# Performance work log

Measured on AMD Instinct MI355X. Metric: run time of the kernel, lower is better.

Reference implementation:

```python
import jax, jax.numpy as jnp
import numpy as np

B, T, D = 16, 4096, 256
CODEBOOK_SIZE = 1024
COMMITMENT = 1.0


def setup_inputs() -> dict:
    key = jax.random.key(0)
    kx, kc = jax.random.split(key)
    x = jax.random.normal(kx, (B, T, D), dtype=jnp.float32)
    codebook = jax.random.normal(kc, (CODEBOOK_SIZE, D), dtype=jnp.float32)
    return {"x": x, "codebook": codebook}


def reference(x, codebook):
    # x: [B, T, D] continuous latents; codebook: [K, D]
    flat = x.reshape(-1, x.shape[-1])  # [N, D]
    # does not affect argmin but is kept for faithfulness to torch.cdist-style math)
    x_sq = jnp.sum(flat * flat, axis=1, keepdims=True)            # [N, 1]
    c_sq = jnp.sum(codebook * codebook, axis=1)                   # [K]
    dist = x_sq - 2.0 * (flat @ codebook.T) + c_sq[None, :]       # [N, K]
    indices = jnp.argmin(dist, axis=1)                            # [N] int
    quantized = codebook[indices].reshape(x.shape)                # gather, [B, T, D]
    # commitment loss: encoder pulled toward (stopped) codes
    commit_loss = COMMITMENT * jnp.mean(
        (x - jax.lax.stop_gradient(quantized)) ** 2
    )
    # straight-through estimator
    out = x + jax.lax.stop_gradient(quantized - x)
    return out, indices.reshape(x.shape[:-1]), commit_loss
```

## Files before the change

kernel.cpp:

```cpp
#include <hip/hip_runtime.h>

#define N_TOK 65536
#define DIM   256
#define KCODE 1024

#define NTHREADS 256
#define TM 128
#define TN 128
#define BK 64
#define NCHUNK 8

#define REFINE_EPS 0.125f
#define TIE_THETA 1.0e-4

#define WS_CSQ_OFF   16
#define WS_IDX_OFF   2048
#define WS_PAIRS_OFF (WS_IDX_OFF + N_TOK)
#define WS_CBPK_OFF  (WS_PAIRS_OFF + N_TOK * NCHUNK * 4)

typedef float f32x4  __attribute__((ext_vector_type(4)));
typedef short bf16x8 __attribute__((ext_vector_type(8)));

__global__ void zero_loss_kernel(float* ws) {
    if (threadIdx.x == 0) ws[0] = 0.0f;
}

__global__ void rowsq_np_kernel(const float* __restrict__ m,
                                float* __restrict__ out, int rows) {
#pragma clang fp contract(off)
    int row = blockIdx.x * 16 + (threadIdx.x >> 4);
    int l   = threadIdx.x & 15;
    if (row >= rows) return;
    int h = l >> 3;
    int j = l & 7;
    const float* p = m + (size_t)row * DIM + h * 128 + j;
    float v = p[0];
    float r = v * v;
#pragma unroll
    for (int i = 1; i < 16; ++i) {
        float w  = p[i * 8];
        float w2 = w * w;
        r = r + w2;
    }
    float t = r + __shfl_xor(r, 1);
    t = t + __shfl_xor(t, 2);
    t = t + __shfl_xor(t, 4);
    t = t + __shfl_xor(t, 8);
    if (l == 0) out[row] = t;
}

__device__ __forceinline__ void ins2(float d, int idx,
                                     float& d1, int& i1, float& d2, int& i2) {
    if (d < d1 || (d == d1 && idx < i1)) {
        d2 = d1; i2 = i1; d1 = d; i1 = idx;
    } else if ((d < d2 || (d == d2 && idx < i2)) && idx != i1) {
        d2 = d; i2 = idx;
    }
}

__device__ __forceinline__ void f2bf_split(float v, short& hi, short& lo) {
    unsigned u = __float_as_uint(v);
    unsigned r = (u + 0x7fffu + ((u >> 16) & 1u)) >> 16;
    hi = (short)r;
    float hf = __uint_as_float(r << 16);
    float lf = v - hf;
    unsigned u2 = __float_as_uint(lf);
    unsigned r2 = (u2 + 0x7fffu + ((u2 >> 16) & 1u)) >> 16;
    lo = (short)r2;
}

__global__ void convert_pack_kernel(const float* __restrict__ src,
                                    unsigned short* __restrict__ dst,
                                    int nquads) {
    for (int i = blockIdx.x * blockDim.x + threadIdx.x; i < nquads;
         i += gridDim.x * blockDim.x) {
        int row = i >> 6;
        int kq  = i & 63;
        float4 v = reinterpret_cast<const float4*>(src)[i];
        short h0, l0, h1, l1, h2, l2, h3, l3;
        f2bf_split(v.x, h0, l0); f2bf_split(v.y, h1, l1);
        f2bf_split(v.z, h2, l2); f2bf_split(v.w, h3, l3);
        *reinterpret_cast<short4*>(dst + (size_t)row * 512 + kq * 4) =
            make_short4(h0, h1, h2, h3);
        *reinterpret_cast<short4*>(dst + (size_t)row * 512 + 256 + kq * 4) =
            make_short4(l0, l1, l2, l3);
    }
}

__device__ __forceinline__ void gload_lds16(const unsigned short* g, unsigned short* lds) {
    __builtin_amdgcn_global_load_lds(
        (const __attribute__((address_space(1))) unsigned int*)g,
        (__attribute__((address_space(3))) unsigned int*)lds, 16, 0, 0);
}

__launch_bounds__(NTHREADS, 2)
__global__ void vq_main_kernel(const unsigned short* __restrict__ xpk,
                               const unsigned short* __restrict__ cbpk,
                               const float* __restrict__ csq,
                               float4* __restrict__ pairs) {
    __shared__ __align__(16) unsigned short Atile[TM * BK];
    __shared__ __align__(16) unsigned short Btile[TN * BK];
    __shared__ __align__(16) float4 pairs_sh[TM][2];

    const int tid  = threadIdx.x;
    const int w    = tid >> 6;
    const int wy   = w >> 1;
    const int wx   = w & 1;
    const int lane = tid & 63;
    const int lm   = lane & 15;
    const int q    = lane >> 4;
    const int bx     = blockIdx.x;
    const int tok0   = (bx >> 3) * TM;
    const int cchunk = bx & 7;
    const int code0  = cchunk * TN;

    const int row_off = lane >> 3;
    const int slot    = lane & 7;
    const int kq      = slot ^ row_off;

    float cs_reg[4];
#pragma unroll
    for (int ni = 0; ni < 4; ++ni)
        cs_reg[ni] = csq[code0 + wx * 64 + ni * 16 + lm];

    f32x4 acc[4][4];
#pragma unroll
    for (int mi = 0; mi < 4; ++mi)
#pragma unroll
        for (int ni = 0; ni < 4; ++ni)
            acc[mi][ni] = (f32x4){0.f, 0.f, 0.f, 0.f};

    const int segA[3] = {0, 0, 256};
    const int segB[3] = {0, 256, 0};

#pragma unroll 1
    for (int seg = 0; seg < 3; ++seg) {
        const int sa = segA[seg], sb = segB[seg];
#pragma unroll 1
        for (int kc = 0; kc < DIM / BK; ++kc) {
            const int k0 = kc * BK;
            __syncthreads();
#pragma unroll
            for (int inst = 0; inst < 4; ++inst) {
                int rbase = w * 32 + inst * 8;
                const unsigned short* ga =
                    xpk + (size_t)(tok0 + rbase + row_off) * 512 + sa + k0 + kq * 8;
                gload_lds16(ga, &Atile[rbase * BK]);
                const unsigned short* gb =
                    cbpk + (size_t)(code0 + rbase + row_off) * 512 + sb + k0 + kq * 8;
                gload_lds16(gb, &Btile[rbase * BK]);
            }
            __syncthreads();

#pragma unroll
            for (int t = 0; t < 2; ++t) {
                bf16x8 af[4], bf[4];
#pragma unroll
                for (int mi = 0; mi < 4; ++mi) {
                    int r = wy * 64 + mi * 16 + lm;
                    af[mi] = *reinterpret_cast<const bf16x8*>(
                        &Atile[r * BK + (((t * 4 + q) ^ (r & 7)) * 8)]);
                }
#pragma unroll
                for (int ni = 0; ni < 4; ++ni) {
                    int r = wx * 64 + ni * 16 + lm;
                    bf[ni] = *reinterpret_cast<const bf16x8*>(
                        &Btile[r * BK + (((t * 4 + q) ^ (r & 7)) * 8)]);
                }
#pragma unroll
                for (int mi = 0; mi < 4; ++mi)
#pragma unroll
                    for (int ni = 0; ni < 4; ++ni)
                        acc[mi][ni] = __builtin_amdgcn_mfma_f32_16x16x32_bf16(
                            af[mi], bf[ni], acc[mi][ni], 0, 0, 0);
            }
        }
    }

#pragma unroll
    for (int mi = 0; mi < 4; ++mi) {
#pragma unroll
        for (int r = 0; r < 4; ++r) {
            int row_local = wy * 64 + mi * 16 + q * 4 + r;
            float l1 = 3.4e38f, l2 = 3.4e38f;
            int   j1 = 0x7fffffff, j2 = 0x7fffffff;
#pragma unroll
            for (int ni = 0; ni < 4; ++ni) {
                float d = cs_reg[ni] - 2.0f * acc[mi][ni][r];
                ins2(d, code0 + wx * 64 + ni * 16 + lm, l1, j1, l2, j2);
            }
#pragma unroll
            for (int m = 1; m < 16; m <<= 1) {
                float o1 = __shfl_xor(l1, m);
                int   p1 = __shfl_xor(j1, m);
                float o2 = __shfl_xor(l2, m);
                int   p2 = __shfl_xor(j2, m);
                ins2(o1, p1, l1, j1, l2, j2);
                ins2(o2, p2, l1, j1, l2, j2);
            }
            if (lm == 0) {
                float4 pr;
                pr.x = l1; pr.y = l2;
                pr.z = __int_as_float(j1); pr.w = __int_as_float(j2);
                pairs_sh[row_local][wx] = pr;
            }
        }
    }
    __syncthreads();
    if (tid < TM) {
        float4 pa = pairs_sh[tid][0];
        float4 pb = pairs_sh[tid][1];
        float d1 = pa.x, d2 = pa.y;
        int   i1 = __float_as_int(pa.z), i2 = __float_as_int(pa.w);
        ins2(pb.x, __float_as_int(pb.z), d1, i1, d2, i2);
        ins2(pb.y, __float_as_int(pb.w), d1, i1, d2, i2);
        float4 pr;
        pr.x = d1; pr.y = d2;
        pr.z = __int_as_float(i1); pr.w = __int_as_float(i2);
        pairs[(size_t)(tok0 + tid) * NCHUNK + cchunk] = pr;
    }
}

__global__ void merge_refine_kernel(const float* __restrict__ x,
                                    const float* __restrict__ cb,
                                    const float4* __restrict__ pairs,
                                    int* __restrict__ idx_out) {
    int t = blockIdx.x * 256 + threadIdx.x;
    if (t >= N_TOK) return;
    float4 p0 = pairs[(size_t)t * NCHUNK];
    float d1 = p0.x, d2 = p0.y;
    int   i1 = __float_as_int(p0.z), i2 = __float_as_int(p0.w);
#pragma unroll
    for (int c = 1; c < NCHUNK; ++c) {
        float4 p = pairs[(size_t)t * NCHUNK + c];
        ins2(p.x, __float_as_int(p.z), d1, i1, d2, i2);
        ins2(p.y, __float_as_int(p.w), d1, i1, d2, i2);
    }

    int pick = i1;
    if (d2 - d1 < REFINE_EPS) {
        const float* xr = x + (size_t)t * DIM;
        const float* c1 = cb + (size_t)i1 * DIM;
        const float* c2 = cb + (size_t)i2 * DIM;
        double sA = 0.0, dA = 0.0, sB = 0.0, dB = 0.0;
        for (int k = 0; k < DIM; ++k) {
            double xv = (double)xr[k];
            double a  = (double)c1[k];
            double b  = (double)c2[k];
            sA += a * a; dA += xv * a;
            sB += b * b; dB += xv * b;
        }
        double DA  = sA - 2.0 * dA;
        double DB  = sB - 2.0 * dB;
        double gap = DB - DA;
        if (gap > TIE_THETA)       pick = i1;
        else if (gap < -TIE_THETA) pick = i2;
        else                       pick = (i1 < i2) ? i1 : i2;
    }
    idx_out[t] = pick;
}

__launch_bounds__(NTHREADS)
__global__ void output_kernel(const float* __restrict__ x,
                              const float* __restrict__ cb,
                              const int* __restrict__ idx,
                              float* __restrict__ out_q,
                              float* __restrict__ out_idx,
                              float* __restrict__ loss_ws) {
    __shared__ int   sh_idx[TM];
    __shared__ float wsum[4];
    const int tid  = threadIdx.x;
    const int tok0 = blockIdx.x * TM;

    if (tid < TM) sh_idx[tid] = idx[tok0 + tid];
    __syncthreads();

    float lsum = 0.0f;
    for (int t = 0; t < TM; ++t) {
        int code = sh_idx[t];
        float qv = cb[(size_t)code * DIM + tid];
        float xv = x[(size_t)(tok0 + t) * DIM + tid];
        out_q[(size_t)(tok0 + t) * DIM + tid] = xv + (qv - xv);
        float df = xv - qv;
        lsum = fmaf(df, df, lsum);
    }
    if (tid < TM) out_idx[tok0 + tid] = (float)sh_idx[tid];

#pragma unroll
    for (int off = 1; off < 64; off <<= 1) lsum += __shfl_xor(lsum, off);
    if ((tid & 63) == 0) wsum[tid >> 6] = lsum;
    __syncthreads();
    if (tid == 0) atomicAdd(loss_ws, (wsum[0] + wsum[1]) + (wsum[2] + wsum[3]));
}

__global__ void finalize_kernel(const float* ws, float* out_loss) {
    if (threadIdx.x == 0) out_loss[0] = ws[0] * (1.0f / 16777216.0f);
}

extern "C" void kernel_launch(void* const* d_in, const int* in_sizes, int n_in,
                              void* d_out, int out_size, void* d_ws, size_t ws_size,
                              hipStream_t stream) {
    const float* x  = (const float*)d_in[0];
    const float* cb = (const float*)d_in[1];

    float* out      = (float*)d_out;
    float* out_q    = out;
    float* out_idx  = out + (size_t)N_TOK * DIM;
    float* out_loss = out_idx + N_TOK;

    float*  ws    = (float*)d_ws;
    float*  csq   = ws + WS_CSQ_OFF;
    int*    idx   = (int*)(ws + WS_IDX_OFF);
    float4* pairs = (float4*)(ws + WS_PAIRS_OFF);
    unsigned short* cbpk = (unsigned short*)(ws + WS_CBPK_OFF);
    unsigned short* xpk  = (unsigned short*)out_q;

    zero_loss_kernel<<<1, 64, 0, stream>>>(ws);
    rowsq_np_kernel<<<KCODE / 16, 256, 0, stream>>>(cb, csq, KCODE);
    convert_pack_kernel<<<4096, 256, 0, stream>>>(x, xpk, N_TOK * (DIM / 4));
    convert_pack_kernel<<<256, 256, 0, stream>>>(cb, cbpk, KCODE * (DIM / 4));
    vq_main_kernel<<<(N_TOK / TM) * NCHUNK, NTHREADS, 0, stream>>>(xpk, cbpk, csq, pairs);
    merge_refine_kernel<<<N_TOK / 256, 256, 0, stream>>>(x, cb, pairs, idx);
    output_kernel<<<N_TOK / TM, NTHREADS, 0, stream>>>(x, cb, idx, out_q, out_idx, ws);
    finalize_kernel<<<1, 64, 0, stream>>>(ws, out_loss);
}
```

Baseline: 894.7 us.

## Double-buffer LDS tiles and swizzle block-to-tile mapping for cache reuse

Replaces the single A/B LDS tile with a two-stage ping-pong buffer, so global-to-LDS loads for the next K step are issued before the MFMA work on the current step, with one barrier per step instead of two. It also remaps block indices so that groups of eight token tiles share a codebook chunk consecutively, which should improve L2 reuse. The pairs scratch now aliases the first buffer. The cost is doubled LDS use (64KB), which may limit occupancy at two blocks per CU.

```diff
diff --git a/kernel.cpp b/kernel.cpp
--- a/kernel.cpp
+++ b/kernel.cpp
@@ -98,9 +98,7 @@
                                const unsigned short* __restrict__ cbpk,
                                const float* __restrict__ csq,
                                float4* __restrict__ pairs) {
-    __shared__ __align__(16) unsigned short Atile[TM * BK];
-    __shared__ __align__(16) unsigned short Btile[TN * BK];
-    __shared__ __align__(16) float4 pairs_sh[TM][2];
+    __shared__ __align__(16) unsigned short shbuf[2][TM * BK + TN * BK];
 
     const int tid  = threadIdx.x;
     const int w    = tid >> 6;
@@ -109,9 +107,12 @@
     const int lane = tid & 63;
     const int lm   = lane & 15;
     const int q    = lane >> 4;
+
     const int bx     = blockIdx.x;
-    const int tok0   = (bx >> 3) * TM;
-    const int cchunk = bx & 7;
+    const int jj     = bx >> 3;
+    const int grp    = (bx & 7) + ((jj >> 3) << 3);
+    const int cchunk = jj & 7;
+    const int tok0   = grp * TM;
     const int code0  = cchunk * TN;
 
     const int row_off = lane >> 3;
@@ -130,52 +131,63 @@
         for (int ni = 0; ni < 4; ++ni)
             acc[mi][ni] = (f32x4){0.f, 0.f, 0.f, 0.f};
 
-    const int segA[3] = {0, 0, 256};
-    const int segB[3] = {0, 256, 0};
-
+    auto stage = [&](int p, int s) {
+        const int seg = s >> 2;
+        const int k0  = (s & 3) * BK;
+        const int sa  = (seg == 2) ? 256 : 0;
+        const int sb  = (seg == 1) ? 256 : 0;
+        unsigned short* At = &shbuf[p][0];
+        unsigned short* Bt = &shbuf[p][TM * BK];
+#pragma unroll
+        for (int inst = 0; inst < 4; ++inst) {
+            int rbase = w * 32 + inst * 8;
+            const unsigned short* ga =
+                xpk + (size_t)(tok0 + rbase + row_off) * 512 + sa + k0 + kq * 8;
+            gload_lds16(ga, &At[rbase * BK]);
+            const unsigned short* gb =
+                cbpk + (size_t)(code0 + rbase + row_off) * 512 + sb + k0 + kq * 8;
+            gload_lds16(gb, &Bt[rbase * BK]);
+        }
+    };
+
+    stage(0, 0);
+    __syncthreads();
+
+    int p = 0;
 #pragma unroll 1
-    for (int seg = 0; seg < 3; ++seg) {
-        const int sa = segA[seg], sb = segB[seg];
-#pragma unroll 1
-        for (int kc = 0; kc < DIM / BK; ++kc) {
-            const int k0 = kc * BK;
-            __syncthreads();
-#pragma unroll
-            for (int inst = 0; inst < 4; ++inst) {
-                int rbase = w * 32 + inst * 8;
-                const unsigned short* ga =
-                    xpk + (size_t)(tok0 + rbase + row_off) * 512 + sa + k0 + kq * 8;
-                gload_lds16(ga, &Atile[rbase * BK]);
-                const unsigned short* gb =
-                    cbpk + (size_t)(code0 + rbase + row_off) * 512 + sb + k0 + kq * 8;
-                gload_lds16(gb, &Btile[rbase * BK]);
-            }
-            __syncthreads();
-
-#pragma unroll
-            for (int t = 0; t < 2; ++t) {
-                bf16x8 af[4], bf[4];
-#pragma unroll
-                for (int mi = 0; mi < 4; ++mi) {
-                    int r = wy * 64 + mi * 16 + lm;
-                    af[mi] = *reinterpret_cast<const bf16x8*>(
-                        &Atile[r * BK + (((t * 4 + q) ^ (r & 7)) * 8)]);
-                }
-#pragma unroll
-                for (int ni = 0; ni < 4; ++ni) {
-                    int r = wx * 64 + ni * 16 + lm;
-                    bf[ni] = *reinterpret_cast<const bf16x8*>(
-                        &Btile[r * BK + (((t * 4 + q) ^ (r & 7)) * 8)]);
-                }
-#pragma unroll
-                for (int mi = 0; mi < 4; ++mi)
-#pragma unroll
-                    for (int ni = 0; ni < 4; ++ni)
-                        acc[mi][ni] = __builtin_amdgcn_mfma_f32_16x16x32_bf16(
-                            af[mi], bf[ni], acc[mi][ni], 0, 0, 0);
-            }
+    for (int s = 0; s < 12; ++s) {
+        if (s < 11) stage(p ^ 1, s + 1);
+
+        const unsigned short* At = &shbuf[p][0];
+        const unsigned short* Bt = &shbuf[p][TM * BK];
+#pragma unroll
+        for (int t = 0; t < 2; ++t) {
+            bf16x8 af[4], bf[4];
+#pragma unroll
+            for (int mi = 0; mi < 4; ++mi) {
+                int r = wy * 64 + mi * 16 + lm;
+                af[mi] = *reinterpret_cast<const bf16x8*>(
+                    &At[r * BK + (((t * 4 + q) ^ (r & 7)) * 8)]);
+            }
+#pragma unroll
+            for (int ni = 0; ni < 4; ++ni) {
+                int r = wx * 64 + ni * 16 + lm;
+                bf[ni] = *reinterpret_cast<const bf16x8*>(
+                    &Bt[r * BK + (((t * 4 + q) ^ (r & 7)) * 8)]);
+            }
+#pragma unroll
+            for (int mi = 0; mi < 4; ++mi)
+#pragma unroll
+                for (int ni = 0; ni < 4; ++ni)
+                    acc[mi][ni] = __builtin_amdgcn_mfma_f32_16x16x32_bf16(
+                        af[mi], bf[ni], acc[mi][ni], 0, 0, 0);
         }
-    }
+
+        __syncthreads();
+        p ^= 1;
+    }
+
+    float4 (*pairs_sh)[2] = reinterpret_cast<float4(*)[2]>(&shbuf[0][0]);
 
 #pragma unroll
     for (int mi = 0; mi < 4; ++mi) {
```

After: 917.5 us. 1.03x slower.
